# Kernel tuning notes

Measured on AMD Instinct MI355X. Metric: run time of the kernel, lower is better.

Reference implementation:

```python
import jax, jax.numpy as jnp
import numpy as np

N = 100_000      # nodes
E = 1_600_000    # edges (avg degree 16)
C_IN = 32
C_OUT = 32


def setup_inputs() -> dict:
    key = jax.random.key(0)
    ks = jax.random.split(key, 8)
    x = jax.random.normal(ks[0], (N, C_IN), jnp.float32)
    edge_index = jax.random.randint(ks[1], (2, E), 0, N)
    edge_weight = jax.random.uniform(ks[2], (E,), jnp.float32)
    h = jax.random.normal(ks[3], (N, C_OUT), jnp.float32)
    s_in = 1.0 / np.sqrt(C_IN)
    s_out = 1.0 / np.sqrt(C_OUT)
    # 6 ChebConvs (gates z, r, h-tilde; each has an x-conv and an h-conv), K=2
    Wx = jax.random.normal(ks[4], (3, 2, C_IN, C_OUT), jnp.float32) * s_in
    bx = jnp.zeros((3, C_OUT), jnp.float32)
    Wh = jax.random.normal(ks[5], (3, 2, C_OUT, C_OUT), jnp.float32) * s_out
    bh = jnp.zeros((3, C_OUT), jnp.float32)
    Wl = jax.random.normal(ks[6], (C_OUT, 1), jnp.float32) * s_out
    bl = jnp.zeros((1,), jnp.float32)
    return dict(x=x, edge_index=edge_index, edge_weight=edge_weight, h=h,
                Wx=Wx, bx=bx, Wh=Wh, bh=bh, Wl=Wl, bl=bl)


def _cheb(v, W, b, coef, src, dst, n):
    # ChebConv, K=2, sym norm, lambda_max=2:
    #   T0 = v ; T1 = Lhat @ v, Lhat = -D^{-1/2} A D^{-1/2} (zero diagonal)
    t1 = jax.ops.segment_sum(coef[:, None] * v[src], dst, num_segments=n)
    return v @ W[0] + t1 @ W[1] + b


def reference(x, edge_index, edge_weight, h, Wx, bx, Wh, bh, Wl, bl):
    n = x.shape[0]
    src, dst = edge_index[0], edge_index[1]
    deg = jax.ops.segment_sum(edge_weight, src, num_segments=n)
    safe = jnp.where(deg > 0, deg, 1.0)
    dis = jnp.where(deg > 0, jax.lax.rsqrt(safe), 0.0)
    coef = -(dis[src] * edge_weight * dis[dst])  # scaled-Laplacian edge coeffs

    def gate(g, v_x, v_h):
        return (_cheb(v_x, Wx[g], bx[g], coef, src, dst, n)
                + _cheb(v_h, Wh[g], bh[g], coef, src, dst, n))

    z = jax.nn.sigmoid(gate(0, x, h))          # update gate
    r = jax.nn.sigmoid(gate(1, x, h))          # reset gate
    h_tilde = jnp.tanh(gate(2, x, h * r))      # candidate state
    h_new = z * h + (1.0 - z) * h_tilde
    out = jax.nn.softplus(jax.nn.relu(h_new) @ Wl + bl)  # [N, 1]
    return (out, h_new)
```

## Files before the change

kernel.cpp:

```cpp
#include <hip/hip_runtime.h>
#include <math.h>

#define NN 100000
#define NE 1600000
#define C  32
#define CAP 48

#define BSH    8
#define BNODES 256
#define NB     392
#define BCAP   4608
#define EPB    4096

#define WQ_SCALE 32767.0f
#define INV_WQ   (1.0f/32767.0f)
#define DEG_FIX  4194304.0f
#define INV_DEG_FIX (1.0f/4194304.0f)

typedef __attribute__((ext_vector_type(8))) short short8;
typedef __attribute__((ext_vector_type(4))) float floatx4;

__device__ __forceinline__ unsigned rn_bf16(float f) {
    unsigned b = __float_as_uint(f);
    return (b + 0x7fffu + ((b >> 16) & 1u)) >> 16;
}

__device__ __forceinline__ float sigm(float a) { return 1.f / (1.f + expf(-a)); }

__device__ __forceinline__ unsigned enc_edge(int s, float w) {
    int wq = (int)(w * WQ_SCALE + 0.5f);
    wq = wq > 32767 ? 32767 : wq;
    return ((unsigned)s << 15) | (unsigned)wq;
}

__device__ __forceinline__ short8 pack_hi8(uint4 a, uint4 b) {
    short8 v;
    v[0] = (short)(a.x >> 16); v[1] = (short)(a.y >> 16);
    v[2] = (short)(a.z >> 16); v[3] = (short)(a.w >> 16);
    v[4] = (short)(b.x >> 16); v[5] = (short)(b.y >> 16);
    v[6] = (short)(b.z >> 16); v[7] = (short)(b.w >> 16);
    return v;
}
__device__ __forceinline__ short8 pack_lo8(uint4 a, uint4 b) {
    short8 v;
    v[0] = (short)(a.x & 0xffffu); v[1] = (short)(a.y & 0xffffu);
    v[2] = (short)(a.z & 0xffffu); v[3] = (short)(a.w & 0xffffu);
    v[4] = (short)(b.x & 0xffffu); v[5] = (short)(b.y & 0xffffu);
    v[6] = (short)(b.z & 0xffffu); v[7] = (short)(b.w & 0xffffu);
    return v;
}

__global__ __launch_bounds__(256) void bin_pass(const int* __restrict__ ei,
                                                const float* __restrict__ w,
                                                int* __restrict__ gbin_d,
                                                int* __restrict__ gbin_s,
                                                uint2* __restrict__ drec,
                                                unsigned* __restrict__ srec) {
    __shared__ int hd[NB], hs[NB], bd[NB], bs[NB];
    int tid = threadIdx.x;
    for (int i = tid; i < NB; i += 256) { hd[i] = 0; hs[i] = 0; }
    __syncthreads();
    int e0 = blockIdx.x * EPB;
    for (int i = tid; i < EPB; i += 256) {
        int e = e0 + i;
        if (e < NE) {
            atomicAdd(&hs[ei[e] >> BSH], 1);
            atomicAdd(&hd[ei[NE + e] >> BSH], 1);
        }
    }
    __syncthreads();
    for (int i = tid; i < NB; i += 256) {
        bd[i] = hd[i] ? atomicAdd(&gbin_d[i], hd[i]) : 0;
        bs[i] = hs[i] ? atomicAdd(&gbin_s[i], hs[i]) : 0;
    }
    __syncthreads();
    for (int i = tid; i < NB; i += 256) { hd[i] = 0; hs[i] = 0; }
    __syncthreads();
    for (int i = tid; i < EPB; i += 256) {
        int e = e0 + i;
        if (e < NE) {
            int s = ei[e], d = ei[NE + e];
            float we = w[e];
            int dbin = d >> BSH;
            int off = bd[dbin] + atomicAdd(&hd[dbin], 1);
            if (off < BCAP)
                drec[(size_t)dbin * BCAP + off] =
                    make_uint2(((unsigned)s << BSH) | (unsigned)(d & (BNODES - 1)),
                               __float_as_uint(we));
            int sbin = s >> BSH;
            int offs = bs[sbin] + atomicAdd(&hs[sbin], 1);
            if (offs < BCAP)
                srec[(size_t)sbin * BCAP + offs] =
                    ((unsigned)(s & (BNODES - 1)) << 22) | (unsigned)(we * DEG_FIX);
        }
    }
}

__global__ __launch_bounds__(256) void bin_build(const uint2* __restrict__ drec,
                                                 const unsigned* __restrict__ srec,
                                                 const int* __restrict__ gbin_d,
                                                 const int* __restrict__ gbin_s,
                                                 unsigned* __restrict__ buckets,
                                                 int* __restrict__ cursor,
                                                 float* __restrict__ dis) {
    __shared__ __align__(16) unsigned lbuck[BNODES * CAP];
    __shared__ int lcur[BNODES];
    __shared__ int ldeg[BNODES];
    int b = blockIdx.x, tid = threadIdx.x;
    if (tid < BNODES) { lcur[tid] = 0; ldeg[tid] = 0; }
    __syncthreads();
    int cnt_d = min(gbin_d[b], BCAP);
    int cnt_s = min(gbin_s[b], BCAP);
    for (int i = tid; i < cnt_d; i += 256) {
        uint2 r = drec[(size_t)b * BCAP + i];
        int d8 = r.x & (BNODES - 1);
        int s  = (int)(r.x >> BSH);
        int pos = atomicAdd(&lcur[d8], 1);
        if (pos < CAP) lbuck[d8 * CAP + pos] = enc_edge(s, __uint_as_float(r.y));
    }
    for (int i = tid; i < cnt_s; i += 256) {
        unsigned r = srec[(size_t)b * BCAP + i];
        atomicAdd(&ldeg[r >> 22], (int)(r & 0x3FFFFFu));
    }
    __syncthreads();
    uint4* gb = (uint4*)(buckets + (size_t)b * BNODES * CAP);
    const uint4* lb = (const uint4*)lbuck;
    for (int i = tid; i < BNODES * CAP / 4; i += 256) gb[i] = lb[i];
    int n = b * BNODES + tid;
    if (tid < BNODES && n < NN) {
        cursor[n] = lcur[tid];
        int di = ldeg[tid];
        dis[n] = di > 0 ? rsqrtf((float)di * INV_DEG_FIX) : 0.f;
    }
}

__global__ __launch_bounds__(256) void build_xh(const float* __restrict__ x,
                                                const float* __restrict__ h,
                                                const float* __restrict__ dis,
                                                unsigned* __restrict__ xh2,
                                                unsigned* __restrict__ xraw2) {
    int t = blockIdx.x * 256 + threadIdx.x;
    if (t >= NN * C) return;
    float d = dis[t >> 5];
    float xv = x[t], hv = h[t];
    xh2[t]   = (rn_bf16(xv * d) << 16) | rn_bf16(hv * d);
    xraw2[t] = (rn_bf16(xv) << 16) | rn_bf16(hv);
}

__global__ __launch_bounds__(256) void agg_xh(const unsigned* __restrict__ buckets,
                                              const int* __restrict__ cursor,
                                              const float* __restrict__ dis,
                                              const unsigned* __restrict__ xh2,
                                              unsigned* __restrict__ agg2) {
    int tid = threadIdx.x;
    int nl = tid >> 5, j = tid & 31;
    int n = blockIdx.x * 8 + nl;
    if (n >= NN) return;
    int cnt = min(cursor[n], CAP);
    float ax0 = 0.f, ax1 = 0.f, ax2 = 0.f, ax3 = 0.f;
    float ah0 = 0.f, ah1 = 0.f, ah2 = 0.f, ah3 = 0.f;
    for (int base = 0; base < cnt; base += 32) {
        int idx = base + j;
        int sv = 0; float cv = 0.f;
        if (idx < cnt) {
            unsigned u = buckets[(size_t)n * CAP + idx];
            sv = (int)(u >> 15);
            cv = (float)(u & 32767u) * INV_WQ;
        }
        int mm = min(32, cnt - base);
        int i2 = 0;
        for (; i2 + 4 <= mm; i2 += 4) {
            int s0 = __shfl(sv, i2 + 0, 32); float c0 = __shfl(cv, i2 + 0, 32);
            int s1 = __shfl(sv, i2 + 1, 32); float c1 = __shfl(cv, i2 + 1, 32);
            int s2 = __shfl(sv, i2 + 2, 32); float c2 = __shfl(cv, i2 + 2, 32);
            int s3 = __shfl(sv, i2 + 3, 32); float c3 = __shfl(cv, i2 + 3, 32);
            unsigned u0 = xh2[(size_t)s0 * C + j];
            unsigned u1 = xh2[(size_t)s1 * C + j];
            unsigned u2 = xh2[(size_t)s2 * C + j];
            unsigned u3 = xh2[(size_t)s3 * C + j];
            ax0 = fmaf(c0, __uint_as_float(u0 & 0xffff0000u), ax0);
            ah0 = fmaf(c0, __uint_as_float(u0 << 16), ah0);
            ax1 = fmaf(c1, __uint_as_float(u1 & 0xffff0000u), ax1);
            ah1 = fmaf(c1, __uint_as_float(u1 << 16), ah1);
            ax2 = fmaf(c2, __uint_as_float(u2 & 0xffff0000u), ax2);
            ah2 = fmaf(c2, __uint_as_float(u2 << 16), ah2);
            ax3 = fmaf(c3, __uint_as_float(u3 & 0xffff0000u), ax3);
            ah3 = fmaf(c3, __uint_as_float(u3 << 16), ah3);
        }
        for (; i2 < mm; ++i2) {
            int s = __shfl(sv, i2, 32); float cf = __shfl(cv, i2, 32);
            unsigned u = xh2[(size_t)s * C + j];
            ax0 = fmaf(cf, __uint_as_float(u & 0xffff0000u), ax0);
            ah0 = fmaf(cf, __uint_as_float(u << 16), ah0);
        }
    }
    float disn = -dis[n];
    float ax = disn * ((ax0 + ax1) + (ax2 + ax3));
    float ah = disn * ((ah0 + ah1) + (ah2 + ah3));
    agg2[(size_t)n * C + j] = (rn_bf16(ax) << 16) | rn_bf16(ah);
}

__global__ __launch_bounds__(256) void gate_mfma(const unsigned* __restrict__ xraw2,
                                                 const unsigned* __restrict__ agg2,
                                                 const float* __restrict__ dis,
                                                 const float* __restrict__ Wx,
                                                 const float* __restrict__ Wh,
                                                 const float* __restrict__ bx,
                                                 const float* __restrict__ bh,
                                                 unsigned* __restrict__ hrz2,
                                                 unsigned short* __restrict__ hr16,
                                                 float* __restrict__ pout) {
    __shared__ __align__(16) unsigned short Bl[20][64][8];
    int tid = threadIdx.x;
    for (int i = tid; i < 20 * 64; i += 256) {
        int f = i >> 6, l = i & 63;
        int t, c;
        if (f < 16) { t = f >> 2; c = f & 3; }
        else        { t = 4 + ((f - 16) >> 1); c = (f - 16) & 1; }
        int g = t >> 1;
        int j = ((t & 1) << 4) + (l & 15);
        int kb = (l >> 4) << 3;
        const float* srcp = (c < 2 ? Wx : Wh) + g * 2048 + (c & 1) * 1024 + j;
        unsigned pk[4];
#pragma unroll
        for (int q = 0; q < 4; ++q) {
            unsigned lo = rn_bf16(srcp[(kb + 2 * q) * 32]);
            unsigned hi = rn_bf16(srcp[(kb + 2 * q + 1) * 32]);
            pk[q] = (hi << 16) | lo;
        }
        *(uint4*)(&Bl[f][l][0]) = make_uint4(pk[0], pk[1], pk[2], pk[3]);
    }

    int lane = tid & 63, wave = tid >> 6;
    int j0 = lane & 15, quad = lane >> 4;
    int tbase = blockIdx.x * 64 + wave * 16;
    int na = tbase + j0;
    short8 A0 = {0,0,0,0,0,0,0,0}, A1 = A0, A2 = A0, A3 = A0;
    if (na < NN) {
        const uint4* px = (const uint4*)(xraw2 + (size_t)na * C + quad * 8);
        uint4 xa = px[0], xb = px[1];
        A0 = pack_hi8(xa, xb);
        A2 = pack_lo8(xa, xb);
        const uint4* pg = (const uint4*)(agg2 + (size_t)na * C + quad * 8);
        uint4 ga = pg[0], gb = pg[1];
        A1 = pack_hi8(ga, gb);
        A3 = pack_lo8(ga, gb);
    }
    __syncthreads();

#define B8(f) (*(const short8*)(&Bl[f][lane][0]))
    floatx4 az0 = {0.f,0.f,0.f,0.f}, az1 = az0, ar0 = az0, ar1 = az0, ap0 = az0, ap1 = az0;
    az0 = __builtin_amdgcn_mfma_f32_16x16x32_bf16(A0, B8(0),  az0, 0, 0, 0);
    az0 = __builtin_amdgcn_mfma_f32_16x16x32_bf16(A1, B8(1),  az0, 0, 0, 0);
    az0 = __builtin_amdgcn_mfma_f32_16x16x32_bf16(A2, B8(2),  az0, 0, 0, 0);
    az0 = __builtin_amdgcn_mfma_f32_16x16x32_bf16(A3, B8(3),  az0, 0, 0, 0);
    az1 = __builtin_amdgcn_mfma_f32_16x16x32_bf16(A0, B8(4),  az1, 0, 0, 0);
    az1 = __builtin_amdgcn_mfma_f32_16x16x32_bf16(A1, B8(5),  az1, 0, 0, 0);
    az1 = __builtin_amdgcn_mfma_f32_16x16x32_bf16(A2, B8(6),  az1, 0, 0, 0);
    az1 = __builtin_amdgcn_mfma_f32_16x16x32_bf16(A3, B8(7),  az1, 0, 0, 0);
    ar0 = __builtin_amdgcn_mfma_f32_16x16x32_bf16(A0, B8(8),  ar0, 0, 0, 0);
    ar0 = __builtin_amdgcn_mfma_f32_16x16x32_bf16(A1, B8(9),  ar0, 0, 0, 0);
    ar0 = __builtin_amdgcn_mfma_f32_16x16x32_bf16(A2, B8(10), ar0, 0, 0, 0);
    ar0 = __builtin_amdgcn_mfma_f32_16x16x32_bf16(A3, B8(11), ar0, 0, 0, 0);
    ar1 = __builtin_amdgcn_mfma_f32_16x16x32_bf16(A0, B8(12), ar1, 0, 0, 0);
    ar1 = __builtin_amdgcn_mfma_f32_16x16x32_bf16(A1, B8(13), ar1, 0, 0, 0);
    ar1 = __builtin_amdgcn_mfma_f32_16x16x32_bf16(A2, B8(14), ar1, 0, 0, 0);
    ar1 = __builtin_amdgcn_mfma_f32_16x16x32_bf16(A3, B8(15), ar1, 0, 0, 0);
    ap0 = __builtin_amdgcn_mfma_f32_16x16x32_bf16(A0, B8(16), ap0, 0, 0, 0);
    ap0 = __builtin_amdgcn_mfma_f32_16x16x32_bf16(A1, B8(17), ap0, 0, 0, 0);
    ap1 = __builtin_amdgcn_mfma_f32_16x16x32_bf16(A0, B8(18), ap1, 0, 0, 0);
    ap1 = __builtin_amdgcn_mfma_f32_16x16x32_bf16(A1, B8(19), ap1, 0, 0, 0);
#undef B8

    float bza = bx[j0]      + bh[j0];
    float bzb = bx[j0 + 16] + bh[j0 + 16];
    float bra = bx[32 + j0] + bh[32 + j0];
    float brb = bx[48 + j0] + bh[48 + j0];
    float bpa = bx[64 + j0] + bh[64 + j0];
    float bpb = bx[80 + j0] + bh[80 + j0];
#pragma unroll
    for (int p = 0; p < 4; ++p) {
        int nr = tbase + quad * 4 + p;
        if (nr >= NN) continue;
        float dn = dis[nr];
        size_t ra = (size_t)nr * C + j0;
        size_t rb = ra + 16;
        float ha = __uint_as_float(xraw2[ra] << 16);
        float hb = __uint_as_float(xraw2[rb] << 16);
        float za  = sigm(az0[p] + bza);
        float zb  = sigm(az1[p] + bzb);
        float rav = sigm(ar0[p] + bra);
        float rbv = sigm(ar1[p] + brb);
        float hra = ha * rav, hrb = hb * rbv;
        hrz2[ra] = (rn_bf16(hra) << 16) | rn_bf16(za);
        hrz2[rb] = (rn_bf16(hrb) << 16) | rn_bf16(zb);
        hr16[ra] = (unsigned short)rn_bf16(dn * hra);
        hr16[rb] = (unsigned short)rn_bf16(dn * hrb);
        pout[ra] = ap0[p] + bpa;
        pout[rb] = ap1[p] + bpb;
    }
}

__global__ __launch_bounds__(256) void final_kernel(const float* __restrict__ h,
                                                    const unsigned* __restrict__ hrz2,
                                                    const float* __restrict__ ph,
                                                    const unsigned* __restrict__ buckets,
                                                    const int* __restrict__ cursor,
                                                    const float* __restrict__ dis,
                                                    const unsigned short* __restrict__ hr16,
                                                    const float* __restrict__ Wh,
                                                    const float* __restrict__ Wl,
                                                    const float* __restrict__ bl,
                                                    float* __restrict__ out,
                                                    float* __restrict__ hnew) {
    __shared__ float sW[2 * 1024];
    __shared__ float sIn[2][8][C];
    int tid = threadIdx.x;
    for (int i = tid; i < 2 * 1024; i += 256) sW[i] = Wh[4096 + i];
    int nl = tid >> 5, j = tid & 31;
    int n = blockIdx.x * 8 + nl;
    if (n >= NN) return;

    int cnt = min(cursor[n], CAP);
    float a0 = 0.f, a1 = 0.f, a2 = 0.f, a3 = 0.f;
    for (int base = 0; base < cnt; base += 32) {
        int idx = base + j;
        int sv = 0; float cv = 0.f;
        if (idx < cnt) {
            unsigned u = buckets[(size_t)n * CAP + idx];
            sv = (int)(u >> 15);
            cv = (float)(u & 32767u) * INV_WQ;
        }
        int mm = min(32, cnt - base);
        int i2 = 0;
        for (; i2 + 4 <= mm; i2 += 4) {
            int s0 = __shfl(sv, i2 + 0, 32); float c0 = __shfl(cv, i2 + 0, 32);
            int s1 = __shfl(sv, i2 + 1, 32); float c1 = __shfl(cv, i2 + 1, 32);
            int s2 = __shfl(sv, i2 + 2, 32); float c2 = __shfl(cv, i2 + 2, 32);
            int s3 = __shfl(sv, i2 + 3, 32); float c3 = __shfl(cv, i2 + 3, 32);
            float v0 = __uint_as_float(((unsigned)hr16[(size_t)s0 * C + j]) << 16);
            float v1 = __uint_as_float(((unsigned)hr16[(size_t)s1 * C + j]) << 16);
            float v2 = __uint_as_float(((unsigned)hr16[(size_t)s2 * C + j]) << 16);
            float v3 = __uint_as_float(((unsigned)hr16[(size_t)s3 * C + j]) << 16);
            a0 = fmaf(c0, v0, a0);
            a1 = fmaf(c1, v1, a1);
            a2 = fmaf(c2, v2, a2);
            a3 = fmaf(c3, v3, a3);
        }
        for (; i2 < mm; ++i2) {
            int s = __shfl(sv, i2, 32); float cf = __shfl(cv, i2, 32);
            a0 = fmaf(cf, __uint_as_float(((unsigned)hr16[(size_t)s * C + j]) << 16), a0);
        }
    }
    float ag = -dis[n] * ((a0 + a1) + (a2 + a3));
    unsigned uz = hrz2[(size_t)n * C + j];
    float hrv = __uint_as_float(uz & 0xffff0000u);
    float zv  = __uint_as_float(uz << 16);
    sIn[0][nl][j] = hrv;
    sIn[1][nl][j] = ag;
    __syncthreads();

    float acc = ph[(size_t)n * C + j];
#pragma unroll
    for (int k = 0; k < C; ++k) {
        int o = k * 32 + j;
        acc = fmaf(sIn[0][nl][k], sW[o], acc);
        acc = fmaf(sIn[1][nl][k], sW[1024 + o], acc);
    }
    float ht = tanhf(acc);
    float hv = h[(size_t)n * C + j];
    float hn = fmaf(zv, hv - ht, ht);
    hnew[(size_t)n * C + j] = hn;
    float p = fmaxf(hn, 0.f) * Wl[j];
#pragma unroll
    for (int off = 16; off; off >>= 1) p += __shfl_down(p, off, 32);
    if (j == 0) {
        float v = p + bl[0];
        out[n] = fmaxf(v, 0.f) + log1pf(expf(-fabsf(v)));
    }
}

extern "C" void kernel_launch(void* const* d_in, const int* in_sizes, int n_in,
                              void* d_out, int out_size, void* d_ws, size_t ws_size,
                              hipStream_t stream) {
    const float* x  = (const float*)d_in[0];
    const int*   ei = (const int*)d_in[1];
    const float* ew = (const float*)d_in[2];
    const float* h  = (const float*)d_in[3];
    const float* Wx = (const float*)d_in[4];
    const float* bx = (const float*)d_in[5];
    const float* Wh = (const float*)d_in[6];
    const float* bh = (const float*)d_in[7];
    const float* Wl = (const float*)d_in[8];
    const float* bl = (const float*)d_in[9];

    float* out  = (float*)d_out;
    float* hnew = out + NN;

    char* ws = (char*)d_ws;
    int*            gbin_d = (int*)ws;
    int*            gbin_s = gbin_d + NB;
    uint2*          drec   = (uint2*)(ws + 4096);
    unsigned*       srec   = (unsigned*)(drec + (size_t)NB * BCAP);
    unsigned*       buckets= srec + (size_t)NB * BCAP;
    int*            cursor = (int*)(buckets + (size_t)NB * BNODES * CAP);
    float*          dis    = (float*)(cursor + NN);
    unsigned*       xh2    = (unsigned*)(dis + NN);
    unsigned*       agg2   = xh2 + (size_t)NN * C;
    float*          pbuf   = (float*)(agg2 + (size_t)NN * C);
    unsigned*       xraw2  = (unsigned*)drec;
    unsigned short* hr16   = (unsigned short*)srec;
    unsigned*       hrz2   = xh2;

    hipMemsetAsync(d_ws, 0, 4096, stream);

    bin_pass    <<<(NE + EPB - 1) / EPB, 256, 0, stream>>>(ei, ew, gbin_d, gbin_s,
                                                           drec, srec);
    bin_build   <<<NB, 256, 0, stream>>>(drec, srec, gbin_d, gbin_s,
                                         buckets, cursor, dis);
    build_xh    <<<(NN * C + 255) / 256, 256, 0, stream>>>(x, h, dis, xh2, xraw2);
    agg_xh      <<<(NN + 7) / 8, 256, 0, stream>>>(buckets, cursor, dis, xh2, agg2);
    gate_mfma   <<<(NN + 63) / 64, 256, 0, stream>>>(xraw2, agg2, dis, Wx, Wh,
                                                     bx, bh, hrz2, hr16, pbuf);
    final_kernel<<<(NN + 7) / 8, 256, 0, stream>>>(h, hrz2, pbuf,
                                                   buckets, cursor, dis, hr16,
                                                   Wh, Wl, bl, out, hnew);
}
```

Before: 281.3 us.

## Stage binned edges in LDS, fuse build_xh into bin_build, unroll gathers by 8

bin_pass now sorts each block's edges by bin in shared memory, using a wave-level prefix scan over the bin histograms. It then writes contiguous runs to the global bin records, which makes the scattered global stores more coalesced. The x/h bf16 packing kernel is folded into bin_build, so dis comes from shared memory and one launch is removed. xraw2 gets its own workspace region because drec is still live at that point. The gather loops in agg_xh and final_kernel are unrolled to 8 outstanding loads to raise memory-level parallelism, at the cost of more registers and a binary search per edge in bin_pass.

```diff
diff --git a/kernel.cpp b/kernel.cpp
--- a/kernel.cpp
+++ b/kernel.cpp
@@ -56,43 +56,73 @@
                                                 int* __restrict__ gbin_s,
                                                 uint2* __restrict__ drec,
                                                 unsigned* __restrict__ srec) {
-    __shared__ int hd[NB], hs[NB], bd[NB], bs[NB];
+    __shared__ int hd[NB], hs[NB];
+    __shared__ int sd[NB], ss[NB];
+    __shared__ int bd[NB], bs[NB];
+    __shared__ int cd[NB], cs[NB];
+    __shared__ __align__(16) uint2 ld[EPB];
+    __shared__ unsigned lsr[EPB];
     int tid = threadIdx.x;
     for (int i = tid; i < NB; i += 256) { hd[i] = 0; hs[i] = 0; }
     __syncthreads();
     int e0 = blockIdx.x * EPB;
-    for (int i = tid; i < EPB; i += 256) {
-        int e = e0 + i;
-        if (e < NE) {
-            atomicAdd(&hs[ei[e] >> BSH], 1);
-            atomicAdd(&hd[ei[NE + e] >> BSH], 1);
-        }
+    int m = min(EPB, NE - e0);
+    for (int i = tid; i < m; i += 256) {
+        atomicAdd(&hs[ei[e0 + i] >> BSH], 1);
+        atomicAdd(&hd[ei[NE + e0 + i] >> BSH], 1);
     }
     __syncthreads();
     for (int i = tid; i < NB; i += 256) {
         bd[i] = hd[i] ? atomicAdd(&gbin_d[i], hd[i]) : 0;
         bs[i] = hs[i] ? atomicAdd(&gbin_s[i], hs[i]) : 0;
     }
-    __syncthreads();
-    for (int i = tid; i < NB; i += 256) { hd[i] = 0; hs[i] = 0; }
-    __syncthreads();
-    for (int i = tid; i < EPB; i += 256) {
-        int e = e0 + i;
-        if (e < NE) {
-            int s = ei[e], d = ei[NE + e];
-            float we = w[e];
-            int dbin = d >> BSH;
-            int off = bd[dbin] + atomicAdd(&hd[dbin], 1);
-            if (off < BCAP)
-                drec[(size_t)dbin * BCAP + off] =
-                    make_uint2(((unsigned)s << BSH) | (unsigned)(d & (BNODES - 1)),
-                               __float_as_uint(we));
-            int sbin = s >> BSH;
-            int offs = bs[sbin] + atomicAdd(&hs[sbin], 1);
-            if (offs < BCAP)
-                srec[(size_t)sbin * BCAP + offs] =
-                    ((unsigned)(s & (BNODES - 1)) << 22) | (unsigned)(we * DEG_FIX);
-        }
+    if (tid < 128) {
+        const int* hh = (tid < 64) ? hd : hs;
+        int* so = (tid < 64) ? sd : ss;
+        int lane = tid & 63;
+        int c0 = lane * 7;
+        int vals[7]; int sum = 0;
+#pragma unroll
+        for (int q = 0; q < 7; ++q) {
+            int idx = c0 + q;
+            int v = (idx < NB) ? hh[idx] : 0;
+            vals[q] = sum; sum += v;
+        }
+        int incl = sum;
+#pragma unroll
+        for (int off = 1; off < 64; off <<= 1) {
+            int t = __shfl_up(incl, off, 64);
+            if (lane >= off) incl += t;
+        }
+        int base = incl - sum;
+#pragma unroll
+        for (int q = 0; q < 7; ++q) {
+            int idx = c0 + q;
+            if (idx < NB) so[idx] = base + vals[q];
+        }
+    }
+    __syncthreads();
+    for (int i = tid; i < NB; i += 256) { cd[i] = sd[i]; cs[i] = ss[i]; }
+    __syncthreads();
+    for (int i = tid; i < m; i += 256) {
+        int s = ei[e0 + i], d = ei[NE + e0 + i];
+        float we = w[e0 + i];
+        int p = atomicAdd(&cd[d >> BSH], 1);
+        ld[p] = make_uint2(((unsigned)s << BSH) | (unsigned)(d & (BNODES - 1)),
+                           __float_as_uint(we));
+        int ps = atomicAdd(&cs[s >> BSH], 1);
+        lsr[ps] = ((unsigned)(s & (BNODES - 1)) << 22) | (unsigned)(we * DEG_FIX);
+    }
+    __syncthreads();
+    for (int i = tid; i < m; i += 256) {
+        int lo = 0, hi = NB - 1;
+        while (lo < hi) { int mid = (lo + hi + 1) >> 1; if (sd[mid] <= i) lo = mid; else hi = mid - 1; }
+        int off = bd[lo] + (i - sd[lo]);
+        if (off < BCAP) drec[(size_t)lo * BCAP + off] = ld[i];
+        lo = 0; hi = NB - 1;
+        while (lo < hi) { int mid = (lo + hi + 1) >> 1; if (ss[mid] <= i) lo = mid; else hi = mid - 1; }
+        off = bs[lo] + (i - ss[lo]);
+        if (off < BCAP) srec[(size_t)lo * BCAP + off] = lsr[i];
     }
 }
 
@@ -100,14 +130,19 @@
                                                  const unsigned* __restrict__ srec,
                                                  const int* __restrict__ gbin_d,
                                                  const int* __restrict__ gbin_s,
+                                                 const float* __restrict__ x,
+                                                 const float* __restrict__ h,
                                                  unsigned* __restrict__ buckets,
                                                  int* __restrict__ cursor,
-                                                 float* __restrict__ dis) {
+                                                 float* __restrict__ dis,
+                                                 unsigned* __restrict__ xh2,
+                                                 unsigned* __restrict__ xraw2) {
     __shared__ __align__(16) unsigned lbuck[BNODES * CAP];
     __shared__ int lcur[BNODES];
     __shared__ int ldeg[BNODES];
+    __shared__ float sdis[BNODES];
     int b = blockIdx.x, tid = threadIdx.x;
-    if (tid < BNODES) { lcur[tid] = 0; ldeg[tid] = 0; }
+    lcur[tid] = 0; ldeg[tid] = 0;
     __syncthreads();
     int cnt_d = min(gbin_d[b], BCAP);
     int cnt_s = min(gbin_s[b], BCAP);
@@ -127,24 +162,25 @@
     const uint4* lb = (const uint4*)lbuck;
     for (int i = tid; i < BNODES * CAP / 4; i += 256) gb[i] = lb[i];
     int n = b * BNODES + tid;
-    if (tid < BNODES && n < NN) {
+    float dv = 0.f;
+    if (n < NN) {
         cursor[n] = lcur[tid];
         int di = ldeg[tid];
-        dis[n] = di > 0 ? rsqrtf((float)di * INV_DEG_FIX) : 0.f;
-    }
-}
-
-__global__ __launch_bounds__(256) void build_xh(const float* __restrict__ x,
-                                                const float* __restrict__ h,
-                                                const float* __restrict__ dis,
-                                                unsigned* __restrict__ xh2,
-                                                unsigned* __restrict__ xraw2) {
-    int t = blockIdx.x * 256 + threadIdx.x;
-    if (t >= NN * C) return;
-    float d = dis[t >> 5];
-    float xv = x[t], hv = h[t];
-    xh2[t]   = (rn_bf16(xv * d) << 16) | rn_bf16(hv * d);
-    xraw2[t] = (rn_bf16(xv) << 16) | rn_bf16(hv);
+        dv = di > 0 ? rsqrtf((float)di * INV_DEG_FIX) : 0.f;
+        dis[n] = dv;
+    }
+    sdis[tid] = dv;
+    __syncthreads();
+    size_t base = (size_t)b * BNODES * C;
+    for (int i = tid; i < BNODES * C; i += 256) {
+        size_t t = base + i;
+        if (t < (size_t)NN * C) {
+            float d = sdis[i >> 5];
+            float xv = x[t], hv = h[t];
+            xh2[t]   = (rn_bf16(xv * d) << 16) | rn_bf16(hv * d);
+            xraw2[t] = (rn_bf16(xv) << 16) | rn_bf16(hv);
+        }
+    }
 }
 
 __global__ __launch_bounds__(256) void agg_xh(const unsigned* __restrict__ buckets,
@@ -169,23 +205,24 @@
         }
         int mm = min(32, cnt - base);
         int i2 = 0;
-        for (; i2 + 4 <= mm; i2 += 4) {
-            int s0 = __shfl(sv, i2 + 0, 32); float c0 = __shfl(cv, i2 + 0, 32);
-            int s1 = __shfl(sv, i2 + 1, 32); float c1 = __shfl(cv, i2 + 1, 32);
-            int s2 = __shfl(sv, i2 + 2, 32); float c2 = __shfl(cv, i2 + 2, 32);
-            int s3 = __shfl(sv, i2 + 3, 32); float c3 = __shfl(cv, i2 + 3, 32);
-            unsigned u0 = xh2[(size_t)s0 * C + j];
-            unsigned u1 = xh2[(size_t)s1 * C + j];
-            unsigned u2 = xh2[(size_t)s2 * C + j];
-            unsigned u3 = xh2[(size_t)s3 * C + j];
-            ax0 = fmaf(c0, __uint_as_float(u0 & 0xffff0000u), ax0);
-            ah0 = fmaf(c0, __uint_as_float(u0 << 16), ah0);
-            ax1 = fmaf(c1, __uint_as_float(u1 & 0xffff0000u), ax1);
-            ah1 = fmaf(c1, __uint_as_float(u1 << 16), ah1);
-            ax2 = fmaf(c2, __uint_as_float(u2 & 0xffff0000u), ax2);
-            ah2 = fmaf(c2, __uint_as_float(u2 << 16), ah2);
-            ax3 = fmaf(c3, __uint_as_float(u3 & 0xffff0000u), ax3);
-            ah3 = fmaf(c3, __uint_as_float(u3 << 16), ah3);
+        for (; i2 + 8 <= mm; i2 += 8) {
+            float vx[8], vh[8], cc[8];
+#pragma unroll
+            for (int q = 0; q < 8; ++q) {
+                int s = __shfl(sv, i2 + q, 32);
+                cc[q] = __shfl(cv, i2 + q, 32);
+                unsigned u = xh2[(size_t)s * C + j];
+                vx[q] = __uint_as_float(u & 0xffff0000u);
+                vh[q] = __uint_as_float(u << 16);
+            }
+            ax0 = fmaf(cc[0], vx[0], ax0); ah0 = fmaf(cc[0], vh[0], ah0);
+            ax1 = fmaf(cc[1], vx[1], ax1); ah1 = fmaf(cc[1], vh[1], ah1);
+            ax2 = fmaf(cc[2], vx[2], ax2); ah2 = fmaf(cc[2], vh[2], ah2);
+            ax3 = fmaf(cc[3], vx[3], ax3); ah3 = fmaf(cc[3], vh[3], ah3);
+            ax0 = fmaf(cc[4], vx[4], ax0); ah0 = fmaf(cc[4], vh[4], ah0);
+            ax1 = fmaf(cc[5], vx[5], ax1); ah1 = fmaf(cc[5], vh[5], ah1);
+            ax2 = fmaf(cc[6], vx[6], ax2); ah2 = fmaf(cc[6], vh[6], ah2);
+            ax3 = fmaf(cc[7], vx[7], ax3); ah3 = fmaf(cc[7], vh[7], ah3);
         }
         for (; i2 < mm; ++i2) {
             int s = __shfl(sv, i2, 32); float cf = __shfl(cv, i2, 32);
@@ -333,19 +370,22 @@
         }
         int mm = min(32, cnt - base);
         int i2 = 0;
-        for (; i2 + 4 <= mm; i2 += 4) {
-            int s0 = __shfl(sv, i2 + 0, 32); float c0 = __shfl(cv, i2 + 0, 32);
-            int s1 = __shfl(sv, i2 + 1, 32); float c1 = __shfl(cv, i2 + 1, 32);
-            int s2 = __shfl(sv, i2 + 2, 32); float c2 = __shfl(cv, i2 + 2, 32);
-            int s3 = __shfl(sv, i2 + 3, 32); float c3 = __shfl(cv, i2 + 3, 32);
-            float v0 = __uint_as_float(((unsigned)hr16[(size_t)s0 * C + j]) << 16);
-            float v1 = __uint_as_float(((unsigned)hr16[(size_t)s1 * C + j]) << 16);
-            float v2 = __uint_as_float(((unsigned)hr16[(size_t)s2 * C + j]) << 16);
-            float v3 = __uint_as_float(((unsigned)hr16[(size_t)s3 * C + j]) << 16);
-            a0 = fmaf(c0, v0, a0);
-            a1 = fmaf(c1, v1, a1);
-            a2 = fmaf(c2, v2, a2);
-            a3 = fmaf(c3, v3, a3);
+        for (; i2 + 8 <= mm; i2 += 8) {
+            float vv[8], cc[8];
+#pragma unroll
+            for (int q = 0; q < 8; ++q) {
+                int s = __shfl(sv, i2 + q, 32);
+                cc[q] = __shfl(cv, i2 + q, 32);
+                vv[q] = __uint_as_float(((unsigned)hr16[(size_t)s * C + j]) << 16);
+            }
+            a0 = fmaf(cc[0], vv[0], a0);
+            a1 = fmaf(cc[1], vv[1], a1);
+            a2 = fmaf(cc[2], vv[2], a2);
+            a3 = fmaf(cc[3], vv[3], a3);
+            a0 = fmaf(cc[4], vv[4], a0);
+            a1 = fmaf(cc[5], vv[5], a1);
+            a2 = fmaf(cc[6], vv[6], a2);
+            a3 = fmaf(cc[7], vv[7], a3);
         }
         for (; i2 < mm; ++i2) {
             int s = __shfl(sv, i2, 32); float cf = __shfl(cv, i2, 32);
@@ -406,9 +446,9 @@
     int*            cursor = (int*)(buckets + (size_t)NB * BNODES * CAP);
     float*          dis    = (float*)(cursor + NN);
     unsigned*       xh2    = (unsigned*)(dis + NN);
-    unsigned*       agg2   = xh2 + (size_t)NN * C;
+    unsigned*       xraw2  = xh2 + (size_t)NN * C;
+    unsigned*       agg2   = xraw2 + (size_t)NN * C;
     float*          pbuf   = (float*)(agg2 + (size_t)NN * C);
-    unsigned*       xraw2  = (unsigned*)drec;
     unsigned short* hr16   = (unsigned short*)srec;
     unsigned*       hrz2   = xh2;
 
@@ -416,9 +456,8 @@
 
     bin_pass    <<<(NE + EPB - 1) / EPB, 256, 0, stream>>>(ei, ew, gbin_d, gbin_s,
                                                            drec, srec);
-    bin_build   <<<NB, 256, 0, stream>>>(drec, srec, gbin_d, gbin_s,
-                                         buckets, cursor, dis);
-    build_xh    <<<(NN * C + 255) / 256, 256, 0, stream>>>(x, h, dis, xh2, xraw2);
+    bin_build   <<<NB, 256, 0, stream>>>(drec, srec, gbin_d, gbin_s, x, h,
+                                         buckets, cursor, dis, xh2, xraw2);
     agg_xh      <<<(NN + 7) / 8, 256, 0, stream>>>(buckets, cursor, dis, xh2, agg2);
     gate_mfma   <<<(NN + 63) / 64, 256, 0, stream>>>(xraw2, agg2, dis, Wx, Wh,
                                                      bx, bh, hrz2, hr16, pbuf);
```

Measured after the change: 302.7 us. +7.6%, slower.
